# Kernel optimization log

Measured on AMD Instinct MI355X. Metric: run time of the kernel, lower is better.

Reference implementation:

```python
import jax, jax.numpy as jnp
import numpy as np


def setup_inputs() -> dict:
    key = jax.random.key(0)
    k1, k2 = jax.random.split(key)
    E, D, N = 1600000, 32, 100000
    e = jax.random.normal(k1, (E, D), dtype=jnp.float32)
    dst = jax.random.randint(k2, (E,), 0, N, dtype=jnp.int64)
    return {"e": e, "dst": dst, "n_nodes": N}


def reference(e, dst, n_nodes):
    # copy_e + mean reducer == segment mean of edge features over dst nodes.
    # DGL yields 0 for nodes with no in-edges.
    sums = jax.ops.segment_sum(e, dst, num_segments=n_nodes)          # [N, D]
    counts = jax.ops.segment_sum(jnp.ones((e.shape[0],), e.dtype), dst,
                                 num_segments=n_nodes)                 # [N]
    denom = jnp.maximum(counts, 1.0)[:, None]
    return sums / denom
```

## Files before the change

### kernel.cpp

```cpp
#include <hip/hip_runtime.h>
#include <hip/hip_bf16.h>


#define D_FEAT 32
#define NPB 64
#define NB_MAX 2048
#define STAGE_MAX 8192
#define CAP_MAX 2048
#define CURSOR_PAD 16

__global__ __launch_bounds__(256) void bucket_bin_kernel(
    const int* __restrict__ dst,
    int* __restrict__ cursor,
    unsigned int* __restrict__ buckets,
    int E, int nb, int cap, int chunk)
{
    __shared__ int hist[NB_MAX];
    __shared__ int offs[NB_MAX];
    __shared__ int run [NB_MAX];
    __shared__ int gpos[NB_MAX];
    __shared__ unsigned int   st_rec[STAGE_MAX];
    __shared__ unsigned short st_b  [STAGE_MAX];
    __shared__ int scan_s[256];

    int t = threadIdx.x;
    int cstart = blockIdx.x * chunk;
    int cn = E - cstart; if (cn > chunk) cn = chunk;
    if (cn <= 0) return;

    for (int i = t; i < nb; i += 256) hist[i] = 0;
    __syncthreads();

    for (int i = t; i < cn; i += 256) {
        int d = dst[cstart + i];
        atomicAdd(&hist[d >> 6], 1);
    }
    __syncthreads();

    int q = (nb + 255) / 256;
    int lo = t * q, hi = lo + q; if (hi > nb) hi = nb;
    int sum = 0;
    for (int i = lo; i < hi; i++) sum += hist[i];
    scan_s[t] = sum;
    __syncthreads();
    for (int off = 1; off < 256; off <<= 1) {
        int v = (t >= off) ? scan_s[t - off] : 0;
        __syncthreads();
        scan_s[t] += v;
        __syncthreads();
    }
    int ex = scan_s[t] - sum;
    for (int i = lo; i < hi; i++) {
        offs[i] = ex;
        run[i]  = ex;
        ex += hist[i];
    }
    __syncthreads();

    for (int i = t; i < nb; i += 256) {
        int h = hist[i];
        gpos[i] = (h > 0) ? atomicAdd(&cursor[i * CURSOR_PAD], h) : 0;
    }

    for (int i = t; i < cn; i += 256) {
        int g = cstart + i;
        int d = dst[g];
        int b = d >> 6;
        int p = atomicAdd(&run[b], 1);
        st_rec[p] = ((unsigned)g << 6) | (unsigned)(d & 63);
        st_b[p]   = (unsigned short)b;
    }
    __syncthreads();

    for (int p = t; p < cn; p += 256) {
        int b = st_b[p];
        int rel = gpos[b] + (p - offs[b]);
        if (rel < cap)
            buckets[(size_t)b * cap + rel] = st_rec[p];
    }
}

__global__ __launch_bounds__(256) void node_sort_kernel(
    const unsigned int* __restrict__ buckets,
    const int* __restrict__ cursor,
    unsigned int* __restrict__ ids2,
    int* __restrict__ startArr,
    int* __restrict__ cntArr,
    int N, int cap)
{
    __shared__ int hist[NPB];
    __shared__ int sc  [NPB];
    __shared__ int run [NPB];
    __shared__ unsigned int st[CAP_MAX];
    int t = threadIdx.x;
    int b = blockIdx.x;

    if (t < NPB) hist[t] = 0;
    __syncthreads();

    int m = cursor[b * CURSOR_PAD]; if (m > cap) m = cap;
    const unsigned int* rec = buckets + (size_t)b * cap;

    for (int i = t; i < m; i += 256)
        atomicAdd(&hist[rec[i] & 63], 1);
    __syncthreads();

    if (t < NPB) sc[t] = hist[t];
    __syncthreads();
    for (int off = 1; off < NPB; off <<= 1) {
        int v = 0;
        if (t < NPB && t >= off) v = sc[t - off];
        __syncthreads();
        if (t < NPB) sc[t] += v;
        __syncthreads();
    }
    if (t < NPB) { sc[t] -= hist[t]; run[t] = sc[t]; }
    __syncthreads();

    for (int i = t; i < m; i += 256) {
        unsigned r = rec[i];
        int p = atomicAdd(&run[r & 63], 1);
        st[p] = r >> 6;
    }
    __syncthreads();

    for (int i = t; i < m; i += 256)
        ids2[(size_t)b * cap + i] = st[i];
    if (t < NPB) {
        int node = b * NPB + t;
        if (node < N) {
            startArr[node] = b * cap + sc[t];
            cntArr[node]   = hist[t];
        }
    }
}

__global__ __launch_bounds__(256) void gather_kernel(
    const float4* __restrict__ e4,
    const unsigned int* __restrict__ ids,
    const int* __restrict__ startArr,
    const int* __restrict__ cntArr,
    float4* __restrict__ out4,
    int N, int fixed_stride)
{
    int node = blockIdx.x * 32 + (threadIdx.x >> 3);
    int j = threadIdx.x & 7;
    if (node >= N) return;
    int c = cntArr[node];
    int s;
    if (fixed_stride > 0) {
        s = node * fixed_stride;
        if (c > fixed_stride) c = fixed_stride;
    } else {
        s = startArr[node];
    }
    float4 a0 = {0.f,0.f,0.f,0.f}, a1 = {0.f,0.f,0.f,0.f};
    float4 a2 = {0.f,0.f,0.f,0.f}, a3 = {0.f,0.f,0.f,0.f};
    int k = 0;
    for (; k + 4 <= c; k += 4) {
        unsigned e0 = ids[s+k], e1 = ids[s+k+1], e2 = ids[s+k+2], e3 = ids[s+k+3];
        float4 v0 = e4[(size_t)e0*8 + j];
        float4 v1 = e4[(size_t)e1*8 + j];
        float4 v2 = e4[(size_t)e2*8 + j];
        float4 v3 = e4[(size_t)e3*8 + j];
        a0.x += v0.x; a0.y += v0.y; a0.z += v0.z; a0.w += v0.w;
        a1.x += v1.x; a1.y += v1.y; a1.z += v1.z; a1.w += v1.w;
        a2.x += v2.x; a2.y += v2.y; a2.z += v2.z; a2.w += v2.w;
        a3.x += v3.x; a3.y += v3.y; a3.z += v3.z; a3.w += v3.w;
    }
    for (; k < c; k++) {
        unsigned e0 = ids[s+k];
        float4 v0 = e4[(size_t)e0*8 + j];
        a0.x += v0.x; a0.y += v0.y; a0.z += v0.z; a0.w += v0.w;
    }
    float inv = 1.0f / (float)(c > 1 ? c : 1);
    float4 r;
    r.x = (a0.x + a1.x + a2.x + a3.x) * inv;
    r.y = (a0.y + a1.y + a2.y + a3.y) * inv;
    r.z = (a0.z + a1.z + a2.z + a3.z) * inv;
    r.w = (a0.w + a1.w + a2.w + a3.w) * inv;
    out4[(size_t)node * 8 + j] = r;
}

#define SLOT_STRIDE 64
__global__ __launch_bounds__(256) void scatter_ids_fixed(
    const int* __restrict__ dst, int* __restrict__ cursor,
    unsigned int* __restrict__ ids, int E)
{
    int i = blockIdx.x * 256 + threadIdx.x;
    if (i >= E) return;
    int d = dst[i];
    int pos = atomicAdd(&cursor[d], 1);
    if (pos < SLOT_STRIDE) ids[d * SLOT_STRIDE + pos] = (unsigned)i;
}

__global__ __launch_bounds__(256) void scatter_atomic_kernel(
    const float4* __restrict__ e4, const int* __restrict__ dst,
    float* __restrict__ sums, int* __restrict__ counts, int total)
{
    int t = blockIdx.x * 256 + threadIdx.x;
    if (t >= total) return;
    int edge = t >> 3;
    int fq = t & 7;
    float4 v = e4[t];
    int d = dst[edge];
    float* o = sums + (size_t)d * D_FEAT + fq * 4;
    atomicAdd(o + 0, v.x);
    atomicAdd(o + 1, v.y);
    atomicAdd(o + 2, v.z);
    atomicAdd(o + 3, v.w);
    if (fq == 0) atomicAdd(counts + d, 1);
}

__global__ __launch_bounds__(256) void finalize_kernel(
    float4* __restrict__ out4, const int* __restrict__ counts, int total)
{
    int t = blockIdx.x * 256 + threadIdx.x;
    if (t >= total) return;
    int node = t >> 3;
    int c = counts[node];
    float inv = 1.0f / (float)(c > 1 ? c : 1);
    float4 v = out4[t];
    v.x *= inv; v.y *= inv; v.z *= inv; v.w *= inv;
    out4[t] = v;
}

extern "C" void kernel_launch(void* const* d_in, const int* in_sizes, int n_in,
                              void* d_out, int out_size, void* d_ws, size_t ws_size,
                              hipStream_t stream) {
    const float4* e4 = (const float4*)d_in[0];
    const int* dst = (const int*)d_in[1];
    int E = in_sizes[0] / D_FEAT;
    int N = out_size / D_FEAT;

    int nb = (N + NPB - 1) / NPB;
    long long avg = (E + nb - 1) / nb;
    long long thresh = avg + 8 * (long long)(__builtin_sqrt((double)avg)) + 64;
    int cap = (int)((thresh + 63) / 64 * 64);

    char* ws = (char*)d_ws;
    size_t fast_need = (size_t)nb * CURSOR_PAD * 4
                     + (size_t)nb * cap * 4 * 2
                     + (size_t)N * 4 * 2;
    size_t r2_need = (size_t)N * 4 + (size_t)N * SLOT_STRIDE * 4;

    if (nb <= NB_MAX && cap <= CAP_MAX && ws_size >= fast_need) {
        int* cursor = (int*)ws;
        unsigned int* buckets = (unsigned int*)(ws + (size_t)nb * CURSOR_PAD * 4);
        unsigned int* ids2 = buckets + (size_t)nb * cap;
        int* startArr = (int*)(ids2 + (size_t)nb * cap);
        int* cntArr = startArr + N;

        hipMemsetAsync(cursor, 0, (size_t)nb * CURSOR_PAD * 4, stream);

        int grid1 = 256;
        int chunk = (E + grid1 - 1) / grid1;
        if (chunk > STAGE_MAX) { grid1 = (E + STAGE_MAX - 1) / STAGE_MAX; chunk = STAGE_MAX; }
        bucket_bin_kernel<<<grid1, 256, 0, stream>>>(dst, cursor, buckets, E, nb, cap, chunk);
        node_sort_kernel<<<nb, 256, 0, stream>>>(buckets, cursor, ids2, startArr, cntArr, N, cap);
        gather_kernel<<<(N + 31) / 32, 256, 0, stream>>>(e4, ids2, startArr, cntArr,
                                                         (float4*)d_out, N, 0);
    } else if (ws_size >= r2_need) {
        int* cursor = (int*)ws;
        unsigned int* ids = (unsigned int*)(ws + (size_t)N * 4);
        hipMemsetAsync(cursor, 0, (size_t)N * 4, stream);
        scatter_ids_fixed<<<(E + 255) / 256, 256, 0, stream>>>(dst, cursor, ids, E);
        gather_kernel<<<(N + 31) / 32, 256, 0, stream>>>(e4, ids, nullptr, cursor,
                                                         (float4*)d_out, N, SLOT_STRIDE);
    } else {
        int* counts = (int*)ws;
        hipMemsetAsync(d_out, 0, (size_t)out_size * sizeof(float), stream);
        hipMemsetAsync(counts, 0, (size_t)N * 4, stream);
        int total = E * (D_FEAT / 4);
        scatter_atomic_kernel<<<(total + 255) / 256, 256, 0, stream>>>(
            e4, dst, (float*)d_out, counts, total);
        int fin = N * (D_FEAT / 4);
        finalize_kernel<<<(fin + 255) / 256, 256, 0, stream>>>(
            (float4*)d_out, counts, fin);
    }
}
```

Measured before the change: 346.6 us.

## Bucket full edge rows by destination block, then reduce in shared memory

Adds a new primary path. One pass bins edges by destination block and copies each full 128-byte feature row, plus a 1-byte local node index, into a per-bucket staging area. A second kernel then streams each bucket contiguously and accumulates per-node sums and counts with shared-memory atomics before writing the mean. This replaces random per-node gathers and the separate node-sort pass with streaming reads, at the cost of an extra full write and read of the edge features and a much larger workspace. The new path runs only if the workspace is big enough; otherwise the old ID-sort-and-gather path is used.

```diff
diff --git a/kernel.cpp b/kernel.cpp
--- a/kernel.cpp
+++ b/kernel.cpp
@@ -5,15 +5,168 @@
 #define D_FEAT 32
 #define NPB 64
 #define NB_MAX 2048
+#define CHUNK 4096
+#define CURSOR_PAD 16
+#define ACC_STRIDE 33
+
+__global__ __launch_bounds__(256) void bin_move_kernel(
+    const int* __restrict__ dst,
+    const float4* __restrict__ e4,
+    int* __restrict__ cursor,
+    float4* __restrict__ rows4,
+    unsigned char* __restrict__ locs,
+    int E, int nb, int cap, int chunk)
+{
+    __shared__ int hist[NB_MAX];
+    __shared__ int offs[NB_MAX];
+    __shared__ int run [NB_MAX];
+    __shared__ unsigned short st_idx [CHUNK];
+    __shared__ unsigned int   st_slot[CHUNK];
+    __shared__ unsigned char  st_loc [CHUNK];
+    __shared__ int scan_s[256];
+
+    int t = threadIdx.x;
+    long long cstart = (long long)blockIdx.x * chunk;
+    long long rem = (long long)E - cstart;
+    int cn = (rem < (long long)chunk) ? (int)rem : chunk;
+    if (cn <= 0) return;
+
+    for (int i = t; i < nb; i += 256) hist[i] = 0;
+    __syncthreads();
+
+    for (int i = t; i < cn; i += 256)
+        atomicAdd(&hist[dst[cstart + i] >> 6], 1);
+    __syncthreads();
+
+    int q = (nb + 255) / 256;
+    int lo = t * q, hi = lo + q; if (hi > nb) hi = nb;
+    int sum = 0;
+    for (int i = lo; i < hi; i++) sum += hist[i];
+    scan_s[t] = sum; __syncthreads();
+    for (int off = 1; off < 256; off <<= 1) {
+        int v = (t >= off) ? scan_s[t - off] : 0;
+        __syncthreads();
+        scan_s[t] += v;
+        __syncthreads();
+    }
+    int ex = scan_s[t] - sum;
+    for (int i = lo; i < hi; i++) { offs[i] = ex; run[i] = ex; ex += hist[i]; }
+    __syncthreads();
+
+    for (int i = t; i < nb; i += 256) {
+        int h = hist[i];
+        int g = (h > 0) ? atomicAdd(&cursor[i * CURSOR_PAD], h) : 0;
+        hist[i] = g - offs[i];
+    }
+    __syncthreads();
+
+    for (int i = t; i < cn; i += 256) {
+        int d = dst[cstart + i];
+        int b = d >> 6;
+        int p = atomicAdd(&run[b], 1);
+        int srel = p + hist[b];
+        st_idx[p] = (unsigned short)i;
+        st_loc[p] = (unsigned char)(d & 63);
+        st_slot[p] = (srel < cap) ? (unsigned)(b * cap + srel) : 0xFFFFFFFFu;
+    }
+    __syncthreads();
+
+    int g8 = t >> 3, j = t & 7;
+    for (int base = 0; base < cn; base += 128) {
+        int p0 = base + g8, p1 = p0 + 32, p2 = p0 + 64, p3 = p0 + 96;
+        bool q0 = p0 < cn, q1 = p1 < cn, q2 = p2 < cn, q3 = p3 < cn;
+        unsigned s0 = q0 ? st_slot[p0] : 0xFFFFFFFFu;
+        unsigned s1 = q1 ? st_slot[p1] : 0xFFFFFFFFu;
+        unsigned s2 = q2 ? st_slot[p2] : 0xFFFFFFFFu;
+        unsigned s3 = q3 ? st_slot[p3] : 0xFFFFFFFFu;
+        int i0 = q0 ? st_idx[p0] : 0, i1 = q1 ? st_idx[p1] : 0;
+        int i2 = q2 ? st_idx[p2] : 0, i3 = q3 ? st_idx[p3] : 0;
+        float4 v0, v1, v2, v3;
+        if (q0) v0 = e4[(size_t)(cstart + i0) * 8 + j];
+        if (q1) v1 = e4[(size_t)(cstart + i1) * 8 + j];
+        if (q2) v2 = e4[(size_t)(cstart + i2) * 8 + j];
+        if (q3) v3 = e4[(size_t)(cstart + i3) * 8 + j];
+        if (s0 != 0xFFFFFFFFu) {
+            rows4[(size_t)s0 * 8 + j] = v0;
+            if (j == 0) locs[s0] = st_loc[p0];
+        }
+        if (s1 != 0xFFFFFFFFu) {
+            rows4[(size_t)s1 * 8 + j] = v1;
+            if (j == 0) locs[s1] = st_loc[p1];
+        }
+        if (s2 != 0xFFFFFFFFu) {
+            rows4[(size_t)s2 * 8 + j] = v2;
+            if (j == 0) locs[s2] = st_loc[p2];
+        }
+        if (s3 != 0xFFFFFFFFu) {
+            rows4[(size_t)s3 * 8 + j] = v3;
+            if (j == 0) locs[s3] = st_loc[p3];
+        }
+    }
+}
+
+__global__ __launch_bounds__(256) void bucket_reduce_kernel(
+    const float4* __restrict__ rows4,
+    const unsigned char* __restrict__ locs,
+    const int* __restrict__ cursor,
+    float4* __restrict__ out4, int N, int cap)
+{
+    __shared__ float acc[NPB * ACC_STRIDE];
+    __shared__ int cnt[NPB];
+    int t = threadIdx.x, b = blockIdx.x;
+    for (int i = t; i < NPB * ACC_STRIDE; i += 256) acc[i] = 0.f;
+    if (t < NPB) cnt[t] = 0;
+    __syncthreads();
+
+    int m = cursor[b * CURSOR_PAD]; if (m > cap) m = cap;
+    size_t rb = (size_t)b * cap;
+    int g8 = t >> 3, j = t & 7;
+
+    for (int base = 0; base < m; base += 64) {
+        int r0 = base + g8, r1 = r0 + 32;
+        bool q0 = r0 < m, q1 = r1 < m;
+        float4 v0, v1; int l0 = 0, l1 = 0;
+        if (q0) { v0 = rows4[(rb + r0) * 8 + j]; l0 = locs[rb + r0]; }
+        if (q1) { v1 = rows4[(rb + r1) * 8 + j]; l1 = locs[rb + r1]; }
+        if (q0) {
+            float* a = &acc[l0 * ACC_STRIDE + j * 4];
+            atomicAdd(a + 0, v0.x); atomicAdd(a + 1, v0.y);
+            atomicAdd(a + 2, v0.z); atomicAdd(a + 3, v0.w);
+            if (j == 0) atomicAdd(&cnt[l0], 1);
+        }
+        if (q1) {
+            float* a = &acc[l1 * ACC_STRIDE + j * 4];
+            atomicAdd(a + 0, v1.x); atomicAdd(a + 1, v1.y);
+            atomicAdd(a + 2, v1.z); atomicAdd(a + 3, v1.w);
+            if (j == 0) atomicAdd(&cnt[l1], 1);
+        }
+    }
+    __syncthreads();
+
+    int node_base = b * NPB;
+    #pragma unroll
+    for (int qq = 0; qq < 2; qq++) {
+        int g = qq * 256 + t;
+        int loc = g >> 3, jq = g & 7;
+        int node = node_base + loc;
+        if (node < N) {
+            int c = cnt[loc];
+            float inv = 1.0f / (float)(c > 1 ? c : 1);
+            const float* a = &acc[loc * ACC_STRIDE + jq * 4];
+            float4 r;
+            r.x = a[0] * inv; r.y = a[1] * inv;
+            r.z = a[2] * inv; r.w = a[3] * inv;
+            out4[(size_t)node * 8 + jq] = r;
+        }
+    }
+}
+
 #define STAGE_MAX 8192
 #define CAP_MAX 2048
-#define CURSOR_PAD 16
 
 __global__ __launch_bounds__(256) void bucket_bin_kernel(
-    const int* __restrict__ dst,
-    int* __restrict__ cursor,
-    unsigned int* __restrict__ buckets,
-    int E, int nb, int cap, int chunk)
+    const int* __restrict__ dst, int* __restrict__ cursor,
+    unsigned int* __restrict__ buckets, int E, int nb, int cap, int chunk)
 {
     __shared__ int hist[NB_MAX];
     __shared__ int offs[NB_MAX];
@@ -22,89 +175,62 @@
     __shared__ unsigned int   st_rec[STAGE_MAX];
     __shared__ unsigned short st_b  [STAGE_MAX];
     __shared__ int scan_s[256];
-
     int t = threadIdx.x;
     int cstart = blockIdx.x * chunk;
     int cn = E - cstart; if (cn > chunk) cn = chunk;
     if (cn <= 0) return;
-
     for (int i = t; i < nb; i += 256) hist[i] = 0;
     __syncthreads();
-
-    for (int i = t; i < cn; i += 256) {
-        int d = dst[cstart + i];
-        atomicAdd(&hist[d >> 6], 1);
-    }
-    __syncthreads();
-
+    for (int i = t; i < cn; i += 256) atomicAdd(&hist[dst[cstart + i] >> 6], 1);
+    __syncthreads();
     int q = (nb + 255) / 256;
     int lo = t * q, hi = lo + q; if (hi > nb) hi = nb;
     int sum = 0;
     for (int i = lo; i < hi; i++) sum += hist[i];
-    scan_s[t] = sum;
-    __syncthreads();
+    scan_s[t] = sum; __syncthreads();
     for (int off = 1; off < 256; off <<= 1) {
         int v = (t >= off) ? scan_s[t - off] : 0;
-        __syncthreads();
-        scan_s[t] += v;
-        __syncthreads();
+        __syncthreads(); scan_s[t] += v; __syncthreads();
     }
     int ex = scan_s[t] - sum;
-    for (int i = lo; i < hi; i++) {
-        offs[i] = ex;
-        run[i]  = ex;
-        ex += hist[i];
-    }
-    __syncthreads();
-
+    for (int i = lo; i < hi; i++) { offs[i] = ex; run[i] = ex; ex += hist[i]; }
+    __syncthreads();
     for (int i = t; i < nb; i += 256) {
         int h = hist[i];
         gpos[i] = (h > 0) ? atomicAdd(&cursor[i * CURSOR_PAD], h) : 0;
     }
-
     for (int i = t; i < cn; i += 256) {
         int g = cstart + i;
         int d = dst[g];
         int b = d >> 6;
         int p = atomicAdd(&run[b], 1);
         st_rec[p] = ((unsigned)g << 6) | (unsigned)(d & 63);
-        st_b[p]   = (unsigned short)b;
-    }
-    __syncthreads();
-
+        st_b[p] = (unsigned short)b;
+    }
+    __syncthreads();
     for (int p = t; p < cn; p += 256) {
         int b = st_b[p];
         int rel = gpos[b] + (p - offs[b]);
-        if (rel < cap)
-            buckets[(size_t)b * cap + rel] = st_rec[p];
+        if (rel < cap) buckets[(size_t)b * cap + rel] = st_rec[p];
     }
 }
 
 __global__ __launch_bounds__(256) void node_sort_kernel(
-    const unsigned int* __restrict__ buckets,
-    const int* __restrict__ cursor,
-    unsigned int* __restrict__ ids2,
-    int* __restrict__ startArr,
-    int* __restrict__ cntArr,
-    int N, int cap)
+    const unsigned int* __restrict__ buckets, const int* __restrict__ cursor,
+    unsigned int* __restrict__ ids2, int* __restrict__ startArr,
+    int* __restrict__ cntArr, int N, int cap)
 {
     __shared__ int hist[NPB];
     __shared__ int sc  [NPB];
     __shared__ int run [NPB];
     __shared__ unsigned int st[CAP_MAX];
-    int t = threadIdx.x;
-    int b = blockIdx.x;
-
+    int t = threadIdx.x, b = blockIdx.x;
     if (t < NPB) hist[t] = 0;
     __syncthreads();
-
     int m = cursor[b * CURSOR_PAD]; if (m > cap) m = cap;
     const unsigned int* rec = buckets + (size_t)b * cap;
-
-    for (int i = t; i < m; i += 256)
-        atomicAdd(&hist[rec[i] & 63], 1);
-    __syncthreads();
-
+    for (int i = t; i < m; i += 256) atomicAdd(&hist[rec[i] & 63], 1);
+    __syncthreads();
     if (t < NPB) sc[t] = hist[t];
     __syncthreads();
     for (int off = 1; off < NPB; off <<= 1) {
@@ -116,70 +242,52 @@
     }
     if (t < NPB) { sc[t] -= hist[t]; run[t] = sc[t]; }
     __syncthreads();
-
     for (int i = t; i < m; i += 256) {
         unsigned r = rec[i];
         int p = atomicAdd(&run[r & 63], 1);
         st[p] = r >> 6;
     }
     __syncthreads();
-
-    for (int i = t; i < m; i += 256)
-        ids2[(size_t)b * cap + i] = st[i];
+    for (int i = t; i < m; i += 256) ids2[(size_t)b * cap + i] = st[i];
     if (t < NPB) {
         int node = b * NPB + t;
-        if (node < N) {
-            startArr[node] = b * cap + sc[t];
-            cntArr[node]   = hist[t];
-        }
+        if (node < N) { startArr[node] = b * cap + sc[t]; cntArr[node] = hist[t]; }
     }
 }
 
 __global__ __launch_bounds__(256) void gather_kernel(
-    const float4* __restrict__ e4,
-    const unsigned int* __restrict__ ids,
-    const int* __restrict__ startArr,
-    const int* __restrict__ cntArr,
-    float4* __restrict__ out4,
-    int N, int fixed_stride)
+    const float4* __restrict__ e4, const unsigned int* __restrict__ ids,
+    const int* __restrict__ startArr, const int* __restrict__ cntArr,
+    float4* __restrict__ out4, int N, int fixed_stride)
 {
     int node = blockIdx.x * 32 + (threadIdx.x >> 3);
     int j = threadIdx.x & 7;
     if (node >= N) return;
     int c = cntArr[node];
     int s;
-    if (fixed_stride > 0) {
-        s = node * fixed_stride;
-        if (c > fixed_stride) c = fixed_stride;
-    } else {
-        s = startArr[node];
-    }
-    float4 a0 = {0.f,0.f,0.f,0.f}, a1 = {0.f,0.f,0.f,0.f};
-    float4 a2 = {0.f,0.f,0.f,0.f}, a3 = {0.f,0.f,0.f,0.f};
+    if (fixed_stride > 0) { s = node * fixed_stride; if (c > fixed_stride) c = fixed_stride; }
+    else s = startArr[node];
+    float4 a0 = {0,0,0,0}, a1 = {0,0,0,0}, a2 = {0,0,0,0}, a3 = {0,0,0,0};
     int k = 0;
     for (; k + 4 <= c; k += 4) {
         unsigned e0 = ids[s+k], e1 = ids[s+k+1], e2 = ids[s+k+2], e3 = ids[s+k+3];
-        float4 v0 = e4[(size_t)e0*8 + j];
-        float4 v1 = e4[(size_t)e1*8 + j];
-        float4 v2 = e4[(size_t)e2*8 + j];
-        float4 v3 = e4[(size_t)e3*8 + j];
-        a0.x += v0.x; a0.y += v0.y; a0.z += v0.z; a0.w += v0.w;
-        a1.x += v1.x; a1.y += v1.y; a1.z += v1.z; a1.w += v1.w;
-        a2.x += v2.x; a2.y += v2.y; a2.z += v2.z; a2.w += v2.w;
-        a3.x += v3.x; a3.y += v3.y; a3.z += v3.z; a3.w += v3.w;
+        float4 v0 = e4[(size_t)e0*8+j], v1 = e4[(size_t)e1*8+j];
+        float4 v2 = e4[(size_t)e2*8+j], v3 = e4[(size_t)e3*8+j];
+        a0.x+=v0.x; a0.y+=v0.y; a0.z+=v0.z; a0.w+=v0.w;
+        a1.x+=v1.x; a1.y+=v1.y; a1.z+=v1.z; a1.w+=v1.w;
+        a2.x+=v2.x; a2.y+=v2.y; a2.z+=v2.z; a2.w+=v2.w;
+        a3.x+=v3.x; a3.y+=v3.y; a3.z+=v3.z; a3.w+=v3.w;
     }
     for (; k < c; k++) {
         unsigned e0 = ids[s+k];
-        float4 v0 = e4[(size_t)e0*8 + j];
-        a0.x += v0.x; a0.y += v0.y; a0.z += v0.z; a0.w += v0.w;
+        float4 v0 = e4[(size_t)e0*8+j];
+        a0.x+=v0.x; a0.y+=v0.y; a0.z+=v0.z; a0.w+=v0.w;
     }
     float inv = 1.0f / (float)(c > 1 ? c : 1);
     float4 r;
-    r.x = (a0.x + a1.x + a2.x + a3.x) * inv;
-    r.y = (a0.y + a1.y + a2.y + a3.y) * inv;
-    r.z = (a0.z + a1.z + a2.z + a3.z) * inv;
-    r.w = (a0.w + a1.w + a2.w + a3.w) * inv;
-    out4[(size_t)node * 8 + j] = r;
+    r.x = (a0.x+a1.x+a2.x+a3.x)*inv; r.y = (a0.y+a1.y+a2.y+a3.y)*inv;
+    r.z = (a0.z+a1.z+a2.z+a3.z)*inv; r.w = (a0.w+a1.w+a2.w+a3.w)*inv;
+    out4[(size_t)node*8+j] = r;
 }
 
 #define SLOT_STRIDE 64
@@ -200,15 +308,11 @@
 {
     int t = blockIdx.x * 256 + threadIdx.x;
     if (t >= total) return;
-    int edge = t >> 3;
-    int fq = t & 7;
+    int edge = t >> 3, fq = t & 7;
     float4 v = e4[t];
     int d = dst[edge];
     float* o = sums + (size_t)d * D_FEAT + fq * 4;
-    atomicAdd(o + 0, v.x);
-    atomicAdd(o + 1, v.y);
-    atomicAdd(o + 2, v.z);
-    atomicAdd(o + 3, v.w);
+    atomicAdd(o+0, v.x); atomicAdd(o+1, v.y); atomicAdd(o+2, v.z); atomicAdd(o+3, v.w);
     if (fq == 0) atomicAdd(counts + d, 1);
 }
 
@@ -225,6 +329,8 @@
     out4[t] = v;
 }
 
+static inline size_t align256(size_t x) { return (x + 255) & ~(size_t)255; }
+
 extern "C" void kernel_launch(void* const* d_in, const int* in_sizes, int n_in,
                               void* d_out, int out_size, void* d_ws, size_t ws_size,
                               hipStream_t stream) {
@@ -239,20 +345,32 @@
     int cap = (int)((thresh + 63) / 64 * 64);
 
     char* ws = (char*)d_ws;
-    size_t fast_need = (size_t)nb * CURSOR_PAD * 4
-                     + (size_t)nb * cap * 4 * 2
-                     + (size_t)N * 4 * 2;
+
+    size_t rows_bytes = (size_t)nb * cap * (D_FEAT * 4);
+    size_t locs_off = align256(rows_bytes);
+    size_t cur_off = align256(locs_off + (size_t)nb * cap);
+    size_t b_need = cur_off + (size_t)nb * CURSOR_PAD * 4;
+
+    size_t r4_need = (size_t)nb * CURSOR_PAD * 4 + (size_t)nb * cap * 4 * 2 + (size_t)N * 8;
     size_t r2_need = (size_t)N * 4 + (size_t)N * SLOT_STRIDE * 4;
 
-    if (nb <= NB_MAX && cap <= CAP_MAX && ws_size >= fast_need) {
+    if (nb <= NB_MAX && ws_size >= b_need) {
+        float4* rows4 = (float4*)ws;
+        unsigned char* locs = (unsigned char*)(ws + locs_off);
+        int* cursor = (int*)(ws + cur_off);
+        hipMemsetAsync(cursor, 0, (size_t)nb * CURSOR_PAD * 4, stream);
+        int grid1 = (E + CHUNK - 1) / CHUNK;
+        bin_move_kernel<<<grid1, 256, 0, stream>>>(dst, e4, cursor, rows4, locs,
+                                                   E, nb, cap, CHUNK);
+        bucket_reduce_kernel<<<nb, 256, 0, stream>>>(rows4, locs, cursor,
+                                                     (float4*)d_out, N, cap);
+    } else if (nb <= NB_MAX && cap <= CAP_MAX && ws_size >= r4_need) {
         int* cursor = (int*)ws;
         unsigned int* buckets = (unsigned int*)(ws + (size_t)nb * CURSOR_PAD * 4);
         unsigned int* ids2 = buckets + (size_t)nb * cap;
         int* startArr = (int*)(ids2 + (size_t)nb * cap);
         int* cntArr = startArr + N;
-
         hipMemsetAsync(cursor, 0, (size_t)nb * CURSOR_PAD * 4, stream);
-
         int grid1 = 256;
         int chunk = (E + grid1 - 1) / grid1;
         if (chunk > STAGE_MAX) { grid1 = (E + STAGE_MAX - 1) / STAGE_MAX; chunk = STAGE_MAX; }
```

Result: slower. 659.2 us (+90.2%).
